# Performance work log

Measured on AMD Instinct MI355X. Metric: run time of the kernel, lower is better.

Reference implementation:

```python
import jax, jax.numpy as jnp
import numpy as np

B, C, H, W = 4, 192, 56, 56


def setup_inputs() -> dict:
    key = jax.random.key(0)
    k1, k2, k3 = jax.random.split(key, 3)
    x = jax.random.normal(k1, (B, C, H, W), dtype=jnp.float32)
    conv_w = jax.random.normal(k2, (C, 2 * C), dtype=jnp.float32) * (1.0 / np.sqrt(2 * C))
    conv_b = jax.random.normal(k3, (C,), dtype=jnp.float32) * 0.01
    bn_gamma = jnp.ones((C,), dtype=jnp.float32)
    bn_beta = jnp.zeros((C,), dtype=jnp.float32)
    bn_mean = jnp.zeros((C,), dtype=jnp.float32)
    bn_var = jnp.ones((C,), dtype=jnp.float32)
    return {"x": x, "conv_w": conv_w, "conv_b": conv_b, "bn_gamma": bn_gamma,
            "bn_beta": bn_beta, "bn_mean": bn_mean, "bn_var": bn_var, "K": 4}


def reference(x, conv_w, conv_b, bn_gamma, bn_beta, bn_mean, bn_var, K):
    b, c, h, w = x.shape
    shifts_h = list(range(0, h, K))          # rolls along H
    shifts_w = list(range(K, w, K))          # rolls along W
    n = len(shifts_h) + len(shifts_w)
    scale = n ** (-0.5)
    # (B, n, C, H, W): all circularly shifted copies (static shift set)
    rolled = jnp.stack([jnp.roll(x, i, axis=2) for i in shifts_h] +
                       [jnp.roll(x, j, axis=3) for j in shifts_w], axis=1)
    # scores: tanh(scale * x * x_rolled), summed over channels -> (B, n, 1, H, W)
    scores = jnp.tanh(rolled * x[:, None] * scale).sum(axis=2, keepdims=True)
    weights = jax.nn.softmax(scores, axis=1)
    out = (rolled * weights).sum(axis=1)     # (B, C, H, W)
    cat = jnp.concatenate([x, out], axis=1)  # (B, 2C, H, W)
    # 1x1 conv as GEMM over channels
    y = jnp.einsum('bchw,oc->bohw', cat, conv_w) + conv_b[None, :, None, None]
    # BatchNorm2d in eval mode (running stats)
    eps = 1e-5
    inv = bn_gamma / jnp.sqrt(bn_var + eps)
    y = (y - bn_mean[None, :, None, None]) * inv[None, :, None, None] + bn_beta[None, :, None, None]
    return jax.nn.gelu(y, approximate=False)
```

## Files before the change

### kernel.cpp

```cpp
#include <hip/hip_runtime.h>
#include <hip/hip_bf16.h>
#include <math.h>

#define BB 4
#define CC 192
#define HH 56
#define WW 56
#define HWW 3136

typedef __attribute__((ext_vector_type(8))) short short8;
typedef __attribute__((ext_vector_type(4))) float f32x4;

__device__ __forceinline__ unsigned short f2b(float f) {
    __hip_bfloat16 h = __float2bfloat16(f);
    return __builtin_bit_cast(unsigned short, h);
}
__device__ __forceinline__ float b2f(unsigned short u) {
    unsigned int x = ((unsigned int)u) << 16;
    return __builtin_bit_cast(float, x);
}

__global__ __launch_bounds__(256) void k_pre(const float* __restrict__ x,
                                             const float* __restrict__ cw,
                                             float* __restrict__ xt,
                                             unsigned short* __restrict__ cwh,
                                             unsigned short* __restrict__ cwl) {
    int tid = threadIdx.x, bid = blockIdx.x;
    if (bid < 2352) {
        __shared__ float tile[32][33];
        int b = bid / 588, rem = bid % 588;
        int by = rem / 98, bx = rem % 98;
        int tx = tid & 31, ty = tid >> 5;
        int p0 = bx * 32, c0 = by * 32;
#pragma unroll
        for (int i = 0; i < 4; i++) {
            int c = c0 + ty + 8 * i;
            tile[ty + 8 * i][tx] = x[(b * CC + c) * HWW + p0 + tx];
        }
        __syncthreads();
#pragma unroll
        for (int i = 0; i < 4; i++) {
            int p = p0 + ty + 8 * i;
            xt[(size_t)(b * HWW + p) * CC + c0 + tx] = tile[tx][ty + 8 * i];
        }
    } else {
        int i = (bid - 2352) * 256 + tid;
        if (i < 384 * 192) {
            int n = i / 192, k = i % 192;
            float v = (n < 192) ? cw[n * 384 + k] : cw[(n - 192) * 384 + 192 + k];
            unsigned short hi = f2b(v);
            cwh[i] = hi;
            cwl[i] = f2b(v - b2f(hi));
        }
    }
}

__global__ __launch_bounds__(256) void k_mid(const float* __restrict__ xt,
                                             const unsigned short* __restrict__ cwh,
                                             const unsigned short* __restrict__ cwl,
                                             float* __restrict__ sp,
                                             float* __restrict__ u,
                                             float* __restrict__ z) {
    __shared__ __align__(16) char smem[36864];
    int tid = threadIdx.x, bid = blockIdx.x;

    if (bid < 1792) {
        float* Xs = (float*)smem;
        const float K2 = 0.38490017945975050f;
        bool isH = bid < 896;
        int lid = isH ? bid : bid - 896;
        int half = lid & 1;
        int rp = (lid >> 1) & 1;
        int cb2 = lid >> 2;
        int b = cb2 / 56, l0 = cb2 % 56;
        int r0 = rp * 2;

        const float* src = xt + (size_t)(b * HWW) * CC + half * 96;
        for (int idx = tid; idx < 28 * 24; idx += 256) {
            int t2 = idx / 24, cq = idx % 24;
            int pi = (r0 + t2 / 14) + 4 * (t2 % 14);
            int pix = isH ? (pi * WW + l0) : (l0 * WW + pi);
            float4 v = *(const float4*)(src + (size_t)pix * CC + cq * 4);
            *(float4*)&Xs[t2 * 100 + cq * 4] = v;
        }
        __syncthreads();

        int perCls = isH ? 105 : 91;
        if (tid < 2 * perCls) {
            int cls = tid / perCls, p = tid % perCls;
            int a, bb;
            if (isH) {
                a = (int)((sqrtf((float)(8 * p + 1)) - 1.0f) * 0.5f);
                bb = p - (a * (a + 1)) / 2;
            } else {
                int ap = (int)((sqrtf((float)(8 * p + 1)) - 1.0f) * 0.5f);
                bb = p - (ap * (ap + 1)) / 2;
                a = ap + 1;
            }
            const float* pA = &Xs[(cls * 14 + a) * 100];
            const float* pB = &Xs[(cls * 14 + bb) * 100];
            float s0 = 0.f, s1 = 0.f, s2 = 0.f, s3 = 0.f;
#pragma unroll
            for (int q = 0; q < 24; q++) {
                float4 av = *(const float4*)(pA + q * 4);
                float4 bv = *(const float4*)(pB + q * 4);
                s0 += __builtin_amdgcn_rcpf(__expf(av.x * bv.x * K2) + 1.0f);
                s1 += __builtin_amdgcn_rcpf(__expf(av.y * bv.y * K2) + 1.0f);
                s2 += __builtin_amdgcn_rcpf(__expf(av.z * bv.z * K2) + 1.0f);
                s3 += __builtin_amdgcn_rcpf(__expf(av.w * bv.w * K2) + 1.0f);
            }
            float s = 96.0f - 2.0f * (s0 + s1 + s2 + s3);
            int r = r0 + cls;
            size_t base = (size_t)(half * BB + b) * HWW;
            if (isH) {
                int i1 = a - bb;
                int h1 = r + 4 * a, h2 = r + 4 * bb;
                sp[(base + h1 * WW + l0) * 32 + i1] = s;
                if (a != bb) sp[(base + h2 * WW + l0) * 32 + (14 - i1)] = s;
            } else {
                int d = a - bb;
                int w1 = r + 4 * a, w2 = r + 4 * bb;
                sp[(base + l0 * WW + w1) * 32 + 14 + (d - 1)] = s;
                sp[(base + l0 * WW + w2) * 32 + 14 + (13 - d)] = s;
            }
        }
        return;
    }

    {
        unsigned short* Ah = (unsigned short*)smem;
        unsigned short* Al = Ah + 64 * 72;
        unsigned short* Bh = Ah + 2 * 64 * 72;
        unsigned short* Bl = Ah + 3 * 64 * 72;
        float* Ds = (float*)smem;
        int vb = bid - 1792;
        int bm = (vb % 196) * 64, bn = (vb / 196) * 64;
        int lane = tid & 63, wv = tid >> 6;

        f32x4 acc[4] = {{0,0,0,0},{0,0,0,0},{0,0,0,0},{0,0,0,0}};

        for (int kc = 0; kc < 3; kc++) {
#pragma unroll
            for (int r2 = 0; r2 < 2; r2++) {
                int idx = tid + r2 * 256;
                int m = idx >> 3, kq = idx & 7;
                const float* s = xt + (size_t)(bm + m) * CC + kc * 64 + kq * 8;
                float4 v0 = *(const float4*)s;
                float4 v1 = *(const float4*)(s + 4);
                float vv[8] = {v0.x, v0.y, v0.z, v0.w, v1.x, v1.y, v1.z, v1.w};
                unsigned short hi[8], lo[8];
#pragma unroll
                for (int e = 0; e < 8; e++) {
                    hi[e] = f2b(vv[e]);
                    lo[e] = f2b(vv[e] - b2f(hi[e]));
                }
                *(short8*)&Ah[m * 72 + kq * 8] = *(short8*)hi;
                *(short8*)&Al[m * 72 + kq * 8] = *(short8*)lo;
                size_t bo = (size_t)(bn + m) * 192 + kc * 64 + kq * 8;
                *(short8*)&Bh[m * 72 + kq * 8] = *(const short8*)(cwh + bo);
                *(short8*)&Bl[m * 72 + kq * 8] = *(const short8*)(cwl + bo);
            }
            __syncthreads();
            int n0 = wv * 16;
            int k8 = lane >> 4;
            int col = lane & 15;
#pragma unroll
            for (int ks = 0; ks < 64; ks += 32) {
                int koff = ks + k8 * 8;
                short8 bfh = *(const short8*)&Bh[(n0 + col) * 72 + koff];
                short8 bfl = *(const short8*)&Bl[(n0 + col) * 72 + koff];
#pragma unroll
                for (int fm = 0; fm < 4; fm++) {
                    short8 afh = *(const short8*)&Ah[(fm * 16 + col) * 72 + koff];
                    short8 afl = *(const short8*)&Al[(fm * 16 + col) * 72 + koff];
                    acc[fm] = __builtin_amdgcn_mfma_f32_16x16x32_bf16(afh, bfh, acc[fm], 0, 0, 0);
                    acc[fm] = __builtin_amdgcn_mfma_f32_16x16x32_bf16(afl, bfh, acc[fm], 0, 0, 0);
                    acc[fm] = __builtin_amdgcn_mfma_f32_16x16x32_bf16(afh, bfl, acc[fm], 0, 0, 0);
                }
            }
            __syncthreads();
        }
        {
            int col = lane & 15, rowq = lane >> 4;
#pragma unroll
            for (int fm = 0; fm < 4; fm++)
#pragma unroll
                for (int rg = 0; rg < 4; rg++)
                    Ds[(fm * 16 + rowq * 4 + rg) * 68 + wv * 16 + col] = acc[fm][rg];
        }
        __syncthreads();
        {
            int c4 = tid & 15, m0 = tid >> 4;
            int cg = bn + c4 * 4;
            float* dst = (cg < 192) ? u : z;
            int cc = (cg < 192) ? cg : cg - 192;
#pragma unroll
            for (int p = 0; p < 4; p++) {
                int m = m0 + p * 16;
                float4 v = *(float4*)&Ds[m * 68 + c4 * 4];
                *(float4*)&dst[(size_t)(bm + m) * CC + cc] = v;
            }
        }
    }
}

__global__ __launch_bounds__(256) void k_soft(const float* __restrict__ sp,
                                              float* __restrict__ wn) {
    int gp = blockIdx.x * 256 + threadIdx.x;
    const float4* p0 = (const float4*)&sp[(size_t)gp * 32];
    const float4* p1 = (const float4*)&sp[((size_t)(4 * HWW) + gp) * 32];
    float sc[28];
#pragma unroll
    for (int j = 0; j < 7; j++) {
        float4 a = p0[j], v = p1[j];
        sc[4 * j + 0] = a.x + v.x; sc[4 * j + 1] = a.y + v.y;
        sc[4 * j + 2] = a.z + v.z; sc[4 * j + 3] = a.w + v.w;
    }
    float mx = -1e30f;
#pragma unroll
    for (int s = 0; s < 27; s++) mx = fmaxf(mx, sc[s]);
    float sum = 0.f;
#pragma unroll
    for (int s = 0; s < 27; s++) { sc[s] = __expf(sc[s] - mx); sum += sc[s]; }
    float inv = __builtin_amdgcn_rcpf(sum);
#pragma unroll
    for (int s = 0; s < 27; s++) sc[s] *= inv;
    sc[27] = 0.f;
    float4* dst = (float4*)(wn + (size_t)gp * 28);
#pragma unroll
    for (int j = 0; j < 7; j++)
        dst[j] = make_float4(sc[4 * j], sc[4 * j + 1], sc[4 * j + 2], sc[4 * j + 3]);
}

__global__ __launch_bounds__(448) void k_accHW(const float* __restrict__ u,
                                               const float* __restrict__ z,
                                               const float* __restrict__ wn,
                                               const float* __restrict__ cb,
                                               const float* __restrict__ gma,
                                               const float* __restrict__ bta,
                                               const float* __restrict__ mea,
                                               const float* __restrict__ var,
                                               float* __restrict__ y) {
    __shared__ float Zs[14 * 56 * 8];
    int tid = threadIdx.x, bid = blockIdx.x;
    int th = bid & 1;
    int t1 = bid >> 1;
    int cc = t1 % 24;
    int t2 = t1 / 24;
    int r = t2 & 3;
    int b = t2 >> 2;
    int w = tid >> 3, c = tid & 7;
    int cg = cc * 8 + c;

#pragma unroll
    for (int it = 0; it < 2; it++) {
        int idx = tid + it * 448;
        if (idx < 784) {
            int t = idx / 56, ww = idx - t * 56;
            const float* s = z + ((size_t)(b * HWW + (r + 4 * t) * WW + ww)) * CC + cc * 8;
            float4 v0 = *(const float4*)s;
            float4 v1 = *(const float4*)(s + 4);
            float* d = &Zs[(t * 56 + ww) * 8];
            *(float4*)d = v0;
            *(float4*)(d + 4) = v1;
        }
    }
    __syncthreads();

    float zc[14];
#pragma unroll
    for (int m = 0; m < 14; m++) {
        int t0 = m + th * 7;
        if (t0 >= 14) t0 -= 14;
        zc[m] = Zs[(t0 * 56 + w) * 8 + c];
    }

    float bias = cb[cg];
    float ginv = gma[cg] * rsqrtf(var[cg] + 1e-5f);
    float bt = bta[cg];
    float me = mea[cg];

    int hbase = r + 4 * (th * 7);
    float acc[7];
#pragma unroll
    for (int tt = 0; tt < 7; tt++) {
        int pix = (hbase + 4 * tt) * WW + w;
        acc[tt] = u[((size_t)(b * HWW + pix)) * CC + cg];
    }

#pragma unroll
    for (int tt = 0; tt < 7; tt++) {
        int t = th * 7 + tt;
        int pix = (hbase + 4 * tt) * WW + w;
        size_t gp = (size_t)b * HWW + pix;
        const float4* wp = (const float4*)(wn + gp * 28);
        float wt[28];
        *(float4*)&wt[0]  = wp[0];
        *(float4*)&wt[4]  = wp[1];
        *(float4*)&wt[8]  = wp[2];
        *(float4*)&wt[12] = wp[3];
        *(float4*)&wt[16] = wp[4];
        *(float4*)&wt[20] = wp[5];
        *(float4*)&wt[24] = wp[6];
        float a = acc[tt];
#pragma unroll
        for (int i = 0; i < 14; i++)
            a += wt[i] * zc[(tt - i + 14) % 14];
#pragma unroll
        for (int j = 1; j <= 13; j++) {
            int wj = w - 4 * j;
            if (wj < 0) wj += 56;
            a += wt[13 + j] * Zs[(t * 56 + wj) * 8 + c];
        }
        float v = (a + bias - me) * ginv + bt;
        v = 0.5f * v * (1.0f + erff(v * 0.70710678118654752f));
        y[((size_t)(b * CC + cg)) * HWW + pix] = v;
    }
}

extern "C" void kernel_launch(void* const* d_in, const int* in_sizes, int n_in,
                              void* d_out, int out_size, void* d_ws, size_t ws_size,
                              hipStream_t stream) {
    const float* x   = (const float*)d_in[0];
    const float* cw  = (const float*)d_in[1];
    const float* cb  = (const float*)d_in[2];
    const float* gma = (const float*)d_in[3];
    const float* bta = (const float*)d_in[4];
    const float* mea = (const float*)d_in[5];
    const float* var = (const float*)d_in[6];
    float* out = (float*)d_out;

    float* ws = (float*)d_ws;
    float*          xt  = ws;
    float*          sp  = ws + 2408448;
    float*          u   = ws + 3211264;
    float*          z   = ws + 5619712;
    float*          wn  = ws + 8028160;
    unsigned short* cwh = (unsigned short*)(ws + 10436608);
    unsigned short* cwl = (unsigned short*)(ws + 10473472);

    k_pre<<<2640, 256, 0, stream>>>(x, cw, xt, cwh, cwl);
    k_mid<<<2968, 256, 0, stream>>>(xt, cwh, cwl, sp, u, z);
    k_soft<<<49, 256, 0, stream>>>(sp, wn);
    k_accHW<<<768, 448, 0, stream>>>(u, z, wn, cb, gma, bta, mea, var, out);
}
```

Baseline: 131.6 us.

## Store transposed input as bf16 hi/lo split and fuse softmax into tail

The pre-pass now writes the transposed input directly as bf16 high/low pairs instead of fp32. The GEMM path loads these without converting, and the score path rebuilds fp32 by adding the two halves. The separate softmax kernel is removed: the tail kernel recomputes max/exp/sum per pixel from the partial scores and applies the normalization after the weighted sum. This saves a launch and a wn round trip, at the cost of softmax work repeated in every channel-group block. The score path also loses a little precision from the hi+lo reconstruction.

```diff
diff --git a/kernel.cpp b/kernel.cpp
--- a/kernel.cpp
+++ b/kernel.cpp
@@ -22,7 +22,8 @@
 
 __global__ __launch_bounds__(256) void k_pre(const float* __restrict__ x,
                                              const float* __restrict__ cw,
-                                             float* __restrict__ xt,
+                                             unsigned short* __restrict__ xth,
+                                             unsigned short* __restrict__ xtl,
                                              unsigned short* __restrict__ cwh,
                                              unsigned short* __restrict__ cwl) {
     int tid = threadIdx.x, bid = blockIdx.x;
@@ -41,7 +42,11 @@
 #pragma unroll
         for (int i = 0; i < 4; i++) {
             int p = p0 + ty + 8 * i;
-            xt[(size_t)(b * HWW + p) * CC + c0 + tx] = tile[tx][ty + 8 * i];
+            float v = tile[tx][ty + 8 * i];
+            unsigned short hi = f2b(v);
+            size_t o = (size_t)(b * HWW + p) * CC + c0 + tx;
+            xth[o] = hi;
+            xtl[o] = f2b(v - b2f(hi));
         }
     } else {
         int i = (bid - 2352) * 256 + tid;
@@ -55,7 +60,8 @@
     }
 }
 
-__global__ __launch_bounds__(256) void k_mid(const float* __restrict__ xt,
+__global__ __launch_bounds__(256) void k_mid(const unsigned short* __restrict__ xth,
+                                             const unsigned short* __restrict__ xtl,
                                              const unsigned short* __restrict__ cwh,
                                              const unsigned short* __restrict__ cwl,
                                              float* __restrict__ sp,
@@ -75,13 +81,20 @@
         int b = cb2 / 56, l0 = cb2 % 56;
         int r0 = rp * 2;
 
-        const float* src = xt + (size_t)(b * HWW) * CC + half * 96;
-        for (int idx = tid; idx < 28 * 24; idx += 256) {
-            int t2 = idx / 24, cq = idx % 24;
+        const unsigned short* srch = xth + (size_t)(b * HWW) * CC + half * 96;
+        const unsigned short* srcl = xtl + (size_t)(b * HWW) * CC + half * 96;
+        for (int idx = tid; idx < 28 * 12; idx += 256) {
+            int t2 = idx / 12, cq = idx % 12;
             int pi = (r0 + t2 / 14) + 4 * (t2 % 14);
             int pix = isH ? (pi * WW + l0) : (l0 * WW + pi);
-            float4 v = *(const float4*)(src + (size_t)pix * CC + cq * 4);
-            *(float4*)&Xs[t2 * 100 + cq * 4] = v;
+            short8 h8 = *(const short8*)(srch + (size_t)pix * CC + cq * 8);
+            short8 l8 = *(const short8*)(srcl + (size_t)pix * CC + cq * 8);
+            float o[8];
+#pragma unroll
+            for (int e = 0; e < 8; e++)
+                o[e] = b2f((unsigned short)h8[e]) + b2f((unsigned short)l8[e]);
+            *(float4*)&Xs[t2 * 100 + cq * 8] = *(float4*)&o[0];
+            *(float4*)&Xs[t2 * 100 + cq * 8 + 4] = *(float4*)&o[4];
         }
         __syncthreads();
 
@@ -144,18 +157,9 @@
             for (int r2 = 0; r2 < 2; r2++) {
                 int idx = tid + r2 * 256;
                 int m = idx >> 3, kq = idx & 7;
-                const float* s = xt + (size_t)(bm + m) * CC + kc * 64 + kq * 8;
-                float4 v0 = *(const float4*)s;
-                float4 v1 = *(const float4*)(s + 4);
-                float vv[8] = {v0.x, v0.y, v0.z, v0.w, v1.x, v1.y, v1.z, v1.w};
-                unsigned short hi[8], lo[8];
-#pragma unroll
-                for (int e = 0; e < 8; e++) {
-                    hi[e] = f2b(vv[e]);
-                    lo[e] = f2b(vv[e] - b2f(hi[e]));
-                }
-                *(short8*)&Ah[m * 72 + kq * 8] = *(short8*)hi;
-                *(short8*)&Al[m * 72 + kq * 8] = *(short8*)lo;
+                size_t ao = (size_t)(bm + m) * CC + kc * 64 + kq * 8;
+                *(short8*)&Ah[m * 72 + kq * 8] = *(const short8*)(xth + ao);
+                *(short8*)&Al[m * 72 + kq * 8] = *(const short8*)(xtl + ao);
                 size_t bo = (size_t)(bn + m) * 192 + kc * 64 + kq * 8;
                 *(short8*)&Bh[m * 72 + kq * 8] = *(const short8*)(cwh + bo);
                 *(short8*)&Bl[m * 72 + kq * 8] = *(const short8*)(cwl + bo);
@@ -204,43 +208,15 @@
     }
 }
 
-__global__ __launch_bounds__(256) void k_soft(const float* __restrict__ sp,
-                                              float* __restrict__ wn) {
-    int gp = blockIdx.x * 256 + threadIdx.x;
-    const float4* p0 = (const float4*)&sp[(size_t)gp * 32];
-    const float4* p1 = (const float4*)&sp[((size_t)(4 * HWW) + gp) * 32];
-    float sc[28];
-#pragma unroll
-    for (int j = 0; j < 7; j++) {
-        float4 a = p0[j], v = p1[j];
-        sc[4 * j + 0] = a.x + v.x; sc[4 * j + 1] = a.y + v.y;
-        sc[4 * j + 2] = a.z + v.z; sc[4 * j + 3] = a.w + v.w;
-    }
-    float mx = -1e30f;
-#pragma unroll
-    for (int s = 0; s < 27; s++) mx = fmaxf(mx, sc[s]);
-    float sum = 0.f;
-#pragma unroll
-    for (int s = 0; s < 27; s++) { sc[s] = __expf(sc[s] - mx); sum += sc[s]; }
-    float inv = __builtin_amdgcn_rcpf(sum);
-#pragma unroll
-    for (int s = 0; s < 27; s++) sc[s] *= inv;
-    sc[27] = 0.f;
-    float4* dst = (float4*)(wn + (size_t)gp * 28);
-#pragma unroll
-    for (int j = 0; j < 7; j++)
-        dst[j] = make_float4(sc[4 * j], sc[4 * j + 1], sc[4 * j + 2], sc[4 * j + 3]);
-}
-
-__global__ __launch_bounds__(448) void k_accHW(const float* __restrict__ u,
-                                               const float* __restrict__ z,
-                                               const float* __restrict__ wn,
-                                               const float* __restrict__ cb,
-                                               const float* __restrict__ gma,
-                                               const float* __restrict__ bta,
-                                               const float* __restrict__ mea,
-                                               const float* __restrict__ var,
-                                               float* __restrict__ y) {
+__global__ __launch_bounds__(448) void k_tail(const float* __restrict__ u,
+                                              const float* __restrict__ z,
+                                              const float* __restrict__ sp,
+                                              const float* __restrict__ cb,
+                                              const float* __restrict__ gma,
+                                              const float* __restrict__ bta,
+                                              const float* __restrict__ mea,
+                                              const float* __restrict__ var,
+                                              float* __restrict__ y) {
     __shared__ float Zs[14 * 56 * 8];
     int tid = threadIdx.x, bid = blockIdx.x;
     int th = bid & 1;
@@ -281,11 +257,11 @@
     float me = mea[cg];
 
     int hbase = r + 4 * (th * 7);
-    float acc[7];
+    float acc0[7];
 #pragma unroll
     for (int tt = 0; tt < 7; tt++) {
         int pix = (hbase + 4 * tt) * WW + w;
-        acc[tt] = u[((size_t)(b * HWW + pix)) * CC + cg];
+        acc0[tt] = u[((size_t)(b * HWW + pix)) * CC + cg];
     }
 
 #pragma unroll
@@ -293,25 +269,36 @@
         int t = th * 7 + tt;
         int pix = (hbase + 4 * tt) * WW + w;
         size_t gp = (size_t)b * HWW + pix;
-        const float4* wp = (const float4*)(wn + gp * 28);
-        float wt[28];
-        *(float4*)&wt[0]  = wp[0];
-        *(float4*)&wt[4]  = wp[1];
-        *(float4*)&wt[8]  = wp[2];
-        *(float4*)&wt[12] = wp[3];
-        *(float4*)&wt[16] = wp[4];
-        *(float4*)&wt[20] = wp[5];
-        *(float4*)&wt[24] = wp[6];
-        float a = acc[tt];
+
+        const float4* p0 = (const float4*)&sp[gp * 32];
+        const float4* p1 = (const float4*)&sp[((size_t)(4 * HWW) + gp) * 32];
+        float sc[28];
+#pragma unroll
+        for (int j = 0; j < 7; j++) {
+            float4 a4 = p0[j], v4 = p1[j];
+            sc[4 * j + 0] = a4.x + v4.x; sc[4 * j + 1] = a4.y + v4.y;
+            sc[4 * j + 2] = a4.z + v4.z; sc[4 * j + 3] = a4.w + v4.w;
+        }
+        float mx = -1e30f;
+#pragma unroll
+        for (int s = 0; s < 27; s++) mx = fmaxf(mx, sc[s]);
+        float sum = 0.f;
+#pragma unroll
+        for (int s = 0; s < 27; s++) { sc[s] = __expf(sc[s] - mx); sum += sc[s]; }
+        float inv = __builtin_amdgcn_rcpf(sum);
+
+        float accw = 0.f;
 #pragma unroll
         for (int i = 0; i < 14; i++)
-            a += wt[i] * zc[(tt - i + 14) % 14];
+            accw += sc[i] * zc[(tt - i + 14) % 14];
 #pragma unroll
         for (int j = 1; j <= 13; j++) {
             int wj = w - 4 * j;
             if (wj < 0) wj += 56;
-            a += wt[13 + j] * Zs[(t * 56 + wj) * 8 + c];
-        }
+            accw += sc[13 + j] * Zs[(t * 56 + wj) * 8 + c];
+        }
+        float a = acc0[tt] + accw * inv;
+
         float v = (a + bias - me) * ginv + bt;
         v = 0.5f * v * (1.0f + erff(v * 0.70710678118654752f));
         y[((size_t)(b * CC + cg)) * HWW + pix] = v;
@@ -331,16 +318,15 @@
     float* out = (float*)d_out;
 
     float* ws = (float*)d_ws;
-    float*          xt  = ws;
-    float*          sp  = ws + 2408448;
-    float*          u   = ws + 3211264;
-    float*          z   = ws + 5619712;
-    float*          wn  = ws + 8028160;
-    unsigned short* cwh = (unsigned short*)(ws + 10436608);
-    unsigned short* cwl = (unsigned short*)(ws + 10473472);
-
-    k_pre<<<2640, 256, 0, stream>>>(x, cw, xt, cwh, cwl);
-    k_mid<<<2968, 256, 0, stream>>>(xt, cwh, cwl, sp, u, z);
-    k_soft<<<49, 256, 0, stream>>>(sp, wn);
-    k_accHW<<<768, 448, 0, stream>>>(u, z, wn, cb, gma, bta, mea, var, out);
-}
+    float*          sp  = ws;
+    float*          u   = ws + 802816;
+    float*          z   = ws + 3211264;
+    unsigned short* xth = (unsigned short*)(ws + 5619712);
+    unsigned short* xtl = (unsigned short*)(ws + 6823936);
+    unsigned short* cwh = (unsigned short*)(ws + 8028160);
+    unsigned short* cwl = (unsigned short*)(ws + 8065024);
+
+    k_pre<<<2640, 256, 0, stream>>>(x, cw, xth, xtl, cwh, cwl);
+    k_mid<<<2968, 256, 0, stream>>>(xth, xtl, cwh, cwl, sp, u, z);
+    k_tail<<<768, 448, 0, stream>>>(u, z, sp, cb, gma, bta, mea, var, out);
+}
```

Result: slower. 135.2 us (+2.7%).
